# Kernel tuning notes

Hardware: AMD Instinct MI355X
Metric: run time of the kernel (lower is better)

The kernel has to match this reference:

```python
import jax, jax.numpy as jnp
import numpy as np


def _dct_last(x):
    """Unnormalized DCT-II along the last axis via the FFT reorder+twiddle trick:
    v[n] = x[2n], v[N-1-n] = x[2n+1];  y[k] = Re( exp(-i*pi*k/(2N)) * FFT(v)[k] )
    => y[k] = sum_n x[n] * cos(pi*(2n+1)*k/(2N))
    This mirrors DREAMPlace's expk (twiddle) formulation.
    """
    N = x.shape[-1]
    v = jnp.concatenate([x[..., ::2], x[..., 1::2][..., ::-1]], axis=-1)
    V = jnp.fft.fft(v)
    k = jnp.arange(N)
    expk = jnp.exp(-1j * jnp.pi * k.astype(x.dtype) / (2.0 * N))
    return jnp.real(V * expk).astype(x.dtype)


def _dct2(x):
    # DCT-II along last axis, then along second-to-last axis (separable 2D DCT).
    y = _dct_last(x)
    y = _dct_last(jnp.swapaxes(y, -1, -2))
    return jnp.swapaxes(y, -1, -2)


def setup_inputs() -> dict:
    key = jax.random.key(0)
    x = jax.random.normal(key, (8, 2048, 2048), dtype=jnp.float32)
    return {"x": x}


def reference(x):
    return _dct2(x)
```

## Files before the change

kernel.cpp:

```cpp
#include <hip/hip_runtime.h>
#include <hip/hip_bf16.h>
#include <hip/hip_fp16.h>


typedef _Float16 half8 __attribute__((ext_vector_type(8)));
typedef float f32x4 __attribute__((ext_vector_type(4)));
typedef unsigned int uint32;

constexpr int TILE_E = 256 * 32;

__device__ __forceinline__ unsigned short f2h_bits(float f) {
  _Float16 h = (_Float16)f;
  return __builtin_bit_cast(unsigned short, h);
}
__device__ __forceinline__ uint32 pk2(float a, float b) {
  return f2h_bits(a) | ((uint32)f2h_bits(b) << 16);
}

__device__ __forceinline__ void gload_lds16(const unsigned short* g, unsigned short* l) {
  __builtin_amdgcn_global_load_lds((const __attribute__((address_space(1))) void*)g,
                                   (__attribute__((address_space(3))) void*)l,
                                   16, 0, 0);
}

#define CFENCE asm volatile("" ::: "memory")

__device__ __forceinline__ int swz_idx(int r, int cbyte) {
  int b = (r >> 1) * 128 + ((((r & 1) << 6) | cbyte) ^ (((r >> 1) & 7) << 4));
  return b >> 1;
}

__device__ __forceinline__ void stage_tile(const unsigned short* __restrict__ G,
                                           int rowbase, int k0, int ld,
                                           unsigned short* lds, int wave, int lane) {
#pragma unroll
  for (int c = 0; c < 2; ++c) {
    const int p = c * 64 + wave * 8 + (lane >> 3);
    const int v = (lane & 7) ^ ((lane >> 3) & 7);
    const int r = 2 * p + (v >> 2);
    const int kslot = v & 3;
    const unsigned short* src = G + (size_t)(rowbase + r) * ld + (k0 + kslot * 8);
    unsigned short* dst = lds + (c * 64 + wave * 8) * 64;
    gload_lds16(src, dst);
  }
}

__global__ __launch_bounds__(256) void cvt_fold22(const float* __restrict__ x,
                                                  unsigned short* __restrict__ Xff) {
  __shared__ float Y[4][2048];
  const int blk = blockIdx.x;
  const int b = blk >> 9;
  const int v = blk & 511;
  const int j = threadIdx.x;
  const float* base = x + (size_t)b * 4194304;
  const float* r0 = base + (size_t)v * 2048;
  const float* r1 = base + (size_t)(2047 - v) * 2048;
  const float* r2 = base + (size_t)(1023 - v) * 2048;
  const float* r3 = base + (size_t)(1024 + v) * 2048;

#pragma unroll
  for (int hh = 0; hh < 2; ++hh) {
    const int c = hh * 1024 + 4 * j;
    float4 a = *(const float4*)(r0 + c);
    float4 bb = *(const float4*)(r1 + c);
    float4 cc = *(const float4*)(r2 + c);
    float4 dd = *(const float4*)(r3 + c);
    float4 sp, sm, d0, d1;
    sp.x = (a.x + bb.x) + (cc.x + dd.x); sm.x = (a.x + bb.x) - (cc.x + dd.x);
    sp.y = (a.y + bb.y) + (cc.y + dd.y); sm.y = (a.y + bb.y) - (cc.y + dd.y);
    sp.z = (a.z + bb.z) + (cc.z + dd.z); sm.z = (a.z + bb.z) - (cc.z + dd.z);
    sp.w = (a.w + bb.w) + (cc.w + dd.w); sm.w = (a.w + bb.w) - (cc.w + dd.w);
    d0.x = a.x - bb.x; d1.x = cc.x - dd.x;
    d0.y = a.y - bb.y; d1.y = cc.y - dd.y;
    d0.z = a.z - bb.z; d1.z = cc.z - dd.z;
    d0.w = a.w - bb.w; d1.w = cc.w - dd.w;
    *(float4*)&Y[0][c] = sp;
    *(float4*)&Y[1][c] = sm;
    *(float4*)&Y[2][c] = d0;
    *(float4*)&Y[3][c] = d1;
  }
  __syncthreads();

  unsigned short* orow[4] = {
      Xff + ((size_t)b * 2048 + v) * 2048,
      Xff + ((size_t)b * 2048 + 512 + v) * 2048,
      Xff + ((size_t)b * 2048 + 1024 + v) * 2048,
      Xff + ((size_t)b * 2048 + 2047 - v) * 2048};
  const int c0 = 8 * j;
  int pA, pD, pB, pC, rng;
  if (j < 64) { rng = 0; pA = 8 * j; pD = 2040 - 8 * j; pB = 1016 - 8 * j; pC = 1024 + 8 * j; }
  else if (j < 128) { rng = 1; pA = 8 * j - 512; pD = 2552 - 8 * j; pB = 1528 - 8 * j; pC = 512 + 8 * j; }
  else { rng = 2; pA = 8 * j - 1024; pD = 3064 - 8 * j; pB = 0; pC = 0; }

#pragma unroll
  for (int t = 0; t < 4; ++t) {
    float val[8];
    float4 a0 = *(const float4*)&Y[t][pA];
    float4 a1 = *(const float4*)&Y[t][pA + 4];
    float4 dd0 = *(const float4*)&Y[t][pD];
    float4 dd1 = *(const float4*)&Y[t][pD + 4];
    const float* A0 = (const float*)&a0;
    const float* A1 = (const float*)&a1;
    const float* D0 = (const float*)&dd0;
    const float* D1 = (const float*)&dd1;
    if (rng == 2) {
#pragma unroll
      for (int e = 0; e < 4; ++e) val[e] = A0[e] - D1[3 - e];
#pragma unroll
      for (int e = 4; e < 8; ++e) val[e] = A1[e - 4] - D0[7 - e];
    } else {
      float4 b0 = *(const float4*)&Y[t][pB];
      float4 b1 = *(const float4*)&Y[t][pB + 4];
      float4 cc0 = *(const float4*)&Y[t][pC];
      float4 cc1 = *(const float4*)&Y[t][pC + 4];
      const float* B0 = (const float*)&b0;
      const float* B1 = (const float*)&b1;
      const float* C0 = (const float*)&cc0;
      const float* C1 = (const float*)&cc1;
#pragma unroll
      for (int e = 0; e < 4; ++e) {
        float P = A0[e] + D1[3 - e];
        float M = B1[3 - e] + C0[e];
        val[e] = rng == 0 ? P + M : P - M;
      }
#pragma unroll
      for (int e = 4; e < 8; ++e) {
        float P = A1[e - 4] + D0[7 - e];
        float M = B0[7 - e] + C1[e - 4];
        val[e] = rng == 0 ? P + M : P - M;
      }
    }
    uint4 o = make_uint4(pk2(val[0], val[1]), pk2(val[2], val[3]),
                         pk2(val[4], val[5]), pk2(val[6], val[7]));
    *(uint4*)(orow[t] + c0) = o;
  }
}

__global__ __launch_bounds__(256) void gen_cos3(unsigned short* __restrict__ C4k,
                                                unsigned short* __restrict__ C2h,
                                                unsigned short* __restrict__ C4h) {
  int idx = blockIdx.x * 256 + threadIdx.x;
  const float s = 7.6699039394282061e-4f;
  if (idx < 1048576) {
    int k = idx >> 10, n = idx & 1023;
    int t = ((2 * n + 1) * (2 * k + 1)) & 8191;
    C4k[idx] = f2h_bits(cosf((float)t * s));
  } else if (idx < 1310720) {
    int i2 = idx - 1048576;
    int k = i2 >> 9, n = i2 & 511;
    int t = ((2 * n + 1) * 4 * k) & 8191;
    C2h[i2] = f2h_bits(cosf((float)t * s));
  } else {
    int i2 = idx - 1310720;
    int k = i2 >> 9, n = i2 & 511;
    int t = ((2 * n + 1) * (4 * k + 2)) & 8191;
    C4h[i2] = f2h_bits(cosf((float)t * s));
  }
}

template <int MODE, int SPLIT>
__global__ __launch_bounds__(512) void dct_gemm(
    const unsigned short* __restrict__ M0, const unsigned short* __restrict__ M1,
    const unsigned short* __restrict__ D, void* __restrict__ outp) {
  constexpr int K = SPLIT ? 512 : 1024;
  constexpr int NT = K / 32;
  __shared__ unsigned short As[4 * TILE_E];
  __shared__ unsigned short Bs[4 * TILE_E];

  const int tid = threadIdx.x;
  const int lane = tid & 63;
  const int wave = tid >> 6;
  const int wr = wave >> 2;
  const int wc = wave & 3;
  const int bmx = blockIdx.y;
  const int bnx = blockIdx.x;
  const int z = blockIdx.z;

  const unsigned short* Ag;
  const unsigned short* Bg;
  int lda, ldb, arow, brow, cls;
  if (MODE == 0) {
    cls = SPLIT ? (bnx >> 1) : 0;
    Ag = D + (SPLIT ? cls * 512 : 1024);
    lda = 2048;
    arow = bmx * 256;
    Bg = SPLIT ? (cls ? M1 : M0) : M0;
    ldb = K;
    brow = (SPLIT ? (bnx & 1) : bnx) * 256;
  } else {
    cls = SPLIT ? (bmx >> 1) : 0;
    Ag = SPLIT ? (cls ? M1 : M0) : M0;
    lda = K;
    arow = (SPLIT ? (bmx & 1) : bmx) * 256;
    Bg = D + (size_t)z * 4194304u + (SPLIT ? cls * 512 : 1024);
    ldb = 2048;
    brow = bnx * 256;
  }

  const int frc = lane & 15;
  const int cb = (lane >> 4) << 4;

  f32x4 acc[8][4] = {};

  stage_tile(Ag, arow, 0, lda, &As[0], wave, lane);
  stage_tile(Bg, brow, 0, ldb, &Bs[0], wave, lane);
  stage_tile(Ag, arow, 32, lda, &As[TILE_E], wave, lane);
  stage_tile(Bg, brow, 32, ldb, &Bs[TILE_E], wave, lane);
  asm volatile("s_waitcnt vmcnt(4)" ::: "memory");
  CFENCE; __builtin_amdgcn_s_barrier(); CFENCE;

  for (int t = 0; t < NT; ++t) {
    const unsigned short* at = &As[(t & 3) * TILE_E];
    const unsigned short* bt = &Bs[(t & 3) * TILE_E];
    half8 af[4], bf[4];

#pragma unroll
    for (int m = 0; m < 4; ++m)
      af[m] = *(const half8*)&at[swz_idx(wr * 128 + m * 16 + frc, cb)];
#pragma unroll
    for (int n = 0; n < 4; ++n)
      bf[n] = *(const half8*)&bt[swz_idx(wc * 64 + n * 16 + frc, cb)];
    if (t + 2 < NT)
      stage_tile(Ag, arow, (t + 2) * 32, lda, &As[((t + 2) & 3) * TILE_E], wave, lane);
    CFENCE; __builtin_amdgcn_s_barrier(); CFENCE;
    __builtin_amdgcn_s_setprio(1);
#pragma unroll
    for (int m = 0; m < 4; ++m)
#pragma unroll
      for (int n = 0; n < 4; ++n)
        acc[m][n] = __builtin_amdgcn_mfma_f32_16x16x32_f16(af[m], bf[n], acc[m][n], 0, 0, 0);
    __builtin_amdgcn_s_setprio(0);

#pragma unroll
    for (int m = 0; m < 4; ++m)
      af[m] = *(const half8*)&at[swz_idx(wr * 128 + 64 + m * 16 + frc, cb)];
    if (t + 2 < NT)
      stage_tile(Bg, brow, (t + 2) * 32, ldb, &Bs[((t + 2) & 3) * TILE_E], wave, lane);
    if (t < NT - 2)
      asm volatile("s_waitcnt vmcnt(4)" ::: "memory");
    else if (t == NT - 2)
      asm volatile("s_waitcnt vmcnt(0)" ::: "memory");
    CFENCE; __builtin_amdgcn_s_barrier(); CFENCE;
    __builtin_amdgcn_s_setprio(1);
#pragma unroll
    for (int m = 0; m < 4; ++m)
#pragma unroll
      for (int n = 0; n < 4; ++n)
        acc[m + 4][n] =
            __builtin_amdgcn_mfma_f32_16x16x32_f16(af[m], bf[n], acc[m + 4][n], 0, 0, 0);
    __builtin_amdgcn_s_setprio(0);
  }

  if (MODE == 0) {
    unsigned short* U2t = (unsigned short*)outp;
#pragma unroll
    for (int mi = 0; mi < 8; ++mi) {
      const int r = arow + wr * 128 + (mi >> 2) * 64 + (mi & 3) * 16 + (lane >> 4) * 4;
      const int b = r >> 11;
      const int rb = r & 2047;
#pragma unroll
      for (int n = 0; n < 4; ++n) {
        const int ccls = brow + wc * 64 + n * 16 + frc;
        const int ktrue = SPLIT ? (4 * ccls + 2 * cls) : (2 * ccls + 1);
        uint32 lo = f2h_bits(acc[mi][n][0]) | ((uint32)f2h_bits(acc[mi][n][1]) << 16);
        uint32 hi = f2h_bits(acc[mi][n][2]) | ((uint32)f2h_bits(acc[mi][n][3]) << 16);
        *(uint2*)&U2t[(size_t)b * 4194304 + (size_t)ktrue * 2048 + rb] =
            make_uint2(lo, hi);
      }
    }
  } else {
    float* out = (float*)outp + (size_t)z * 4194304;
#pragma unroll
    for (int mi = 0; mi < 8; ++mi) {
      const int p0 = arow + wr * 128 + (mi >> 2) * 64 + (mi & 3) * 16 + (lane >> 4) * 4;
#pragma unroll
      for (int n = 0; n < 4; ++n) {
        const int cg = brow + wc * 64 + n * 16 + frc;
#pragma unroll
        for (int i = 0; i < 4; ++i) {
          const int rtrue = SPLIT ? (4 * (p0 + i) + 2 * cls) : (2 * (p0 + i) + 1);
          out[(size_t)rtrue * 2048 + cg] = acc[mi][n][i];
        }
      }
    }
  }
}

extern "C" void kernel_launch(void* const* d_in, const int* in_sizes, int n_in,
                              void* d_out, int out_size, void* d_ws,
                              size_t ws_size, hipStream_t stream) {
  const float* x = (const float*)d_in[0];
  float* out = (float*)d_out;

  unsigned short* Xff = (unsigned short*)d_ws;
  unsigned short* C4k = Xff + 33554432u;
  unsigned short* C2h = C4k + 1048576u;
  unsigned short* C4h = C2h + 262144u;
  unsigned short* U2t = C4h + 262144u;

  cvt_fold22<<<4096, 256, 0, stream>>>(x, Xff);
  gen_cos3<<<6144, 256, 0, stream>>>(C4k, C2h, C4h);
  dct_gemm<0, 0><<<dim3(4, 64, 1), 512, 0, stream>>>(C4k, C4k, Xff, (void*)U2t);
  dct_gemm<0, 1><<<dim3(4, 64, 1), 512, 0, stream>>>(C2h, C4h, Xff, (void*)U2t);
  dct_gemm<1, 0><<<dim3(8, 4, 8), 512, 0, stream>>>(C4k, C4k, U2t, (void*)out);
  dct_gemm<1, 1><<<dim3(8, 4, 8), 512, 0, stream>>>(C2h, C4h, U2t, (void*)out);
}
```

Before: 199.1 us.

## Shrink GEMM tiles to 128x128 and drop the multi-buffered LDS pipeline

Replaces the 256x256-tile, 512-thread GEMM that staged tiles through a 4-deep LDS ring with a 128x128-tile, 256-thread kernel. This kernel loads each K-slice and waits on __syncthreads before computing, with no prefetch. The grid grows fourfold, which adds blocks and occupancy but lowers operand reuse per block. Because global loads no longer overlap with MFMA work, latency is exposed on every K step.

Result: slower. 225.4 us (+13.2%).

```diff
diff --git a/kernel.cpp b/kernel.cpp
--- a/kernel.cpp
+++ b/kernel.cpp
@@ -6,8 +6,6 @@
 typedef _Float16 half8 __attribute__((ext_vector_type(8)));
 typedef float f32x4 __attribute__((ext_vector_type(4)));
 typedef unsigned int uint32;
-
-constexpr int TILE_E = 256 * 32;
 
 __device__ __forceinline__ unsigned short f2h_bits(float f) {
   _Float16 h = (_Float16)f;
@@ -23,25 +21,22 @@
                                    16, 0, 0);
 }
 
-#define CFENCE asm volatile("" ::: "memory")
-
 __device__ __forceinline__ int swz_idx(int r, int cbyte) {
   int b = (r >> 1) * 128 + ((((r & 1) << 6) | cbyte) ^ (((r >> 1) & 7) << 4));
   return b >> 1;
 }
 
-__device__ __forceinline__ void stage_tile(const unsigned short* __restrict__ G,
-                                           int rowbase, int k0, int ld,
-                                           unsigned short* lds, int wave, int lane) {
+__device__ __forceinline__ void stage_tile128(const unsigned short* __restrict__ G,
+                                              int rowbase, int k0, int ld,
+                                              unsigned short* lds, int wave, int lane) {
 #pragma unroll
   for (int c = 0; c < 2; ++c) {
-    const int p = c * 64 + wave * 8 + (lane >> 3);
+    const int p = c * 32 + wave * 8 + (lane >> 3);
     const int v = (lane & 7) ^ ((lane >> 3) & 7);
     const int r = 2 * p + (v >> 2);
     const int kslot = v & 3;
-    const unsigned short* src = G + (size_t)(rowbase + r) * ld + (k0 + kslot * 8);
-    unsigned short* dst = lds + (c * 64 + wave * 8) * 64;
-    gload_lds16(src, dst);
+    gload_lds16(G + (size_t)(rowbase + r) * ld + (k0 + kslot * 8),
+                lds + (c * 32 + wave * 8) * 64);
   }
 }
 
@@ -159,19 +154,19 @@
 }
 
 template <int MODE, int SPLIT>
-__global__ __launch_bounds__(512) void dct_gemm(
+__global__ __launch_bounds__(256) void dct_gemm(
     const unsigned short* __restrict__ M0, const unsigned short* __restrict__ M1,
     const unsigned short* __restrict__ D, void* __restrict__ outp) {
   constexpr int K = SPLIT ? 512 : 1024;
   constexpr int NT = K / 32;
-  __shared__ unsigned short As[4 * TILE_E];
-  __shared__ unsigned short Bs[4 * TILE_E];
+  __shared__ unsigned short As[4096];
+  __shared__ unsigned short Bs[4096];
 
   const int tid = threadIdx.x;
   const int lane = tid & 63;
   const int wave = tid >> 6;
-  const int wr = wave >> 2;
-  const int wc = wave & 3;
+  const int wr = wave >> 1;
+  const int wc = wave & 1;
   const int bmx = blockIdx.y;
   const int bnx = blockIdx.x;
   const int z = blockIdx.z;
@@ -180,82 +175,53 @@
   const unsigned short* Bg;
   int lda, ldb, arow, brow, cls;
   if (MODE == 0) {
-    cls = SPLIT ? (bnx >> 1) : 0;
+    cls = SPLIT ? (bnx >> 2) : 0;
     Ag = D + (SPLIT ? cls * 512 : 1024);
     lda = 2048;
-    arow = bmx * 256;
+    arow = bmx * 128;
     Bg = SPLIT ? (cls ? M1 : M0) : M0;
     ldb = K;
-    brow = (SPLIT ? (bnx & 1) : bnx) * 256;
+    brow = (SPLIT ? (bnx & 3) : bnx) * 128;
   } else {
-    cls = SPLIT ? (bmx >> 1) : 0;
+    cls = SPLIT ? (bmx >> 2) : 0;
     Ag = SPLIT ? (cls ? M1 : M0) : M0;
     lda = K;
-    arow = (SPLIT ? (bmx & 1) : bmx) * 256;
+    arow = (SPLIT ? (bmx & 3) : bmx) * 128;
     Bg = D + (size_t)z * 4194304u + (SPLIT ? cls * 512 : 1024);
     ldb = 2048;
-    brow = bnx * 256;
+    brow = bnx * 128;
   }
 
   const int frc = lane & 15;
   const int cb = (lane >> 4) << 4;
 
-  f32x4 acc[8][4] = {};
-
-  stage_tile(Ag, arow, 0, lda, &As[0], wave, lane);
-  stage_tile(Bg, brow, 0, ldb, &Bs[0], wave, lane);
-  stage_tile(Ag, arow, 32, lda, &As[TILE_E], wave, lane);
-  stage_tile(Bg, brow, 32, ldb, &Bs[TILE_E], wave, lane);
-  asm volatile("s_waitcnt vmcnt(4)" ::: "memory");
-  CFENCE; __builtin_amdgcn_s_barrier(); CFENCE;
+  f32x4 acc[4][4] = {};
 
   for (int t = 0; t < NT; ++t) {
-    const unsigned short* at = &As[(t & 3) * TILE_E];
-    const unsigned short* bt = &Bs[(t & 3) * TILE_E];
+    stage_tile128(Ag, arow, t * 32, lda, As, wave, lane);
+    stage_tile128(Bg, brow, t * 32, ldb, Bs, wave, lane);
+    __syncthreads();
+
     half8 af[4], bf[4];
-
 #pragma unroll
     for (int m = 0; m < 4; ++m)
-      af[m] = *(const half8*)&at[swz_idx(wr * 128 + m * 16 + frc, cb)];
+      af[m] = *(const half8*)&As[swz_idx(wr * 64 + m * 16 + frc, cb)];
 #pragma unroll
     for (int n = 0; n < 4; ++n)
-      bf[n] = *(const half8*)&bt[swz_idx(wc * 64 + n * 16 + frc, cb)];
-    if (t + 2 < NT)
-      stage_tile(Ag, arow, (t + 2) * 32, lda, &As[((t + 2) & 3) * TILE_E], wave, lane);
-    CFENCE; __builtin_amdgcn_s_barrier(); CFENCE;
-    __builtin_amdgcn_s_setprio(1);
+      bf[n] = *(const half8*)&Bs[swz_idx(wc * 64 + n * 16 + frc, cb)];
 #pragma unroll
     for (int m = 0; m < 4; ++m)
 #pragma unroll
       for (int n = 0; n < 4; ++n)
         acc[m][n] = __builtin_amdgcn_mfma_f32_16x16x32_f16(af[m], bf[n], acc[m][n], 0, 0, 0);
-    __builtin_amdgcn_s_setprio(0);
-
-#pragma unroll
-    for (int m = 0; m < 4; ++m)
-      af[m] = *(const half8*)&at[swz_idx(wr * 128 + 64 + m * 16 + frc, cb)];
-    if (t + 2 < NT)
-      stage_tile(Bg, brow, (t + 2) * 32, ldb, &Bs[((t + 2) & 3) * TILE_E], wave, lane);
-    if (t < NT - 2)
-      asm volatile("s_waitcnt vmcnt(4)" ::: "memory");
-    else if (t == NT - 2)
-      asm volatile("s_waitcnt vmcnt(0)" ::: "memory");
-    CFENCE; __builtin_amdgcn_s_barrier(); CFENCE;
-    __builtin_amdgcn_s_setprio(1);
-#pragma unroll
-    for (int m = 0; m < 4; ++m)
-#pragma unroll
-      for (int n = 0; n < 4; ++n)
-        acc[m + 4][n] =
-            __builtin_amdgcn_mfma_f32_16x16x32_f16(af[m], bf[n], acc[m + 4][n], 0, 0, 0);
-    __builtin_amdgcn_s_setprio(0);
+    __syncthreads();
   }
 
   if (MODE == 0) {
     unsigned short* U2t = (unsigned short*)outp;
 #pragma unroll
-    for (int mi = 0; mi < 8; ++mi) {
-      const int r = arow + wr * 128 + (mi >> 2) * 64 + (mi & 3) * 16 + (lane >> 4) * 4;
+    for (int mi = 0; mi < 4; ++mi) {
+      const int r = arow + wr * 64 + mi * 16 + (lane >> 4) * 4;
       const int b = r >> 11;
       const int rb = r & 2047;
 #pragma unroll
@@ -271,8 +237,8 @@
   } else {
     float* out = (float*)outp + (size_t)z * 4194304;
 #pragma unroll
-    for (int mi = 0; mi < 8; ++mi) {
-      const int p0 = arow + wr * 128 + (mi >> 2) * 64 + (mi & 3) * 16 + (lane >> 4) * 4;
+    for (int mi = 0; mi < 4; ++mi) {
+      const int p0 = arow + wr * 64 + mi * 16 + (lane >> 4) * 4;
 #pragma unroll
       for (int n = 0; n < 4; ++n) {
         const int cg = brow + wc * 64 + n * 16 + frc;
@@ -300,8 +266,8 @@
 
   cvt_fold22<<<4096, 256, 0, stream>>>(x, Xff);
   gen_cos3<<<6144, 256, 0, stream>>>(C4k, C2h, C4h);
-  dct_gemm<0, 0><<<dim3(4, 64, 1), 512, 0, stream>>>(C4k, C4k, Xff, (void*)U2t);
-  dct_gemm<0, 1><<<dim3(4, 64, 1), 512, 0, stream>>>(C2h, C4h, Xff, (void*)U2t);
-  dct_gemm<1, 0><<<dim3(8, 4, 8), 512, 0, stream>>>(C4k, C4k, U2t, (void*)out);
-  dct_gemm<1, 1><<<dim3(8, 4, 8), 512, 0, stream>>>(C2h, C4h, U2t, (void*)out);
-}
+  dct_gemm<0, 0><<<dim3(8, 128, 1), 256, 0, stream>>>(C4k, C4k, Xff, (void*)U2t);
+  dct_gemm<0, 1><<<dim3(8, 128, 1), 256, 0, stream>>>(C2h, C4h, Xff, (void*)U2t);
+  dct_gemm<1, 0><<<dim3(16, 8, 8), 256, 0, stream>>>(C4k, C4k, U2t, (void*)out);
+  dct_gemm<1, 1><<<dim3(16, 8, 8), 256, 0, stream>>>(C2h, C4h, U2t, (void*)out);
+}
```
